# Performance work log

Hardware: AMD Instinct MI355X
Metric: run time of the kernel (lower is better)

Reference implementation:

```python
import jax, jax.numpy as jnp
import numpy as np

STATE_SIZE = 29
ACTION_SIZE = 3


def setup_inputs() -> dict:
    key = jax.random.key(0)
    ks = jax.random.split(key, 12)

    def row_norm(k, shape, scale=1.0):
        w = jax.random.normal(k, shape, dtype=jnp.float32)
        return w * (scale / jnp.sqrt(jnp.sum(w * w, axis=1, keepdims=True)))

    lrelu_gain = float(np.sqrt(2.0 / (1.0 + 0.01 ** 2)))  # torch calculate_gain('leaky_relu')
    inp = {
        "x": jax.random.normal(ks[0], (1, STATE_SIZE), dtype=jnp.float32),
        "hx": jnp.zeros((1, 128), jnp.float32),
        "cx": jnp.zeros((1, 128), jnp.float32),
        "w1": row_norm(ks[1], (256, STATE_SIZE)) * lrelu_gain,
        "b1": jnp.zeros((256,), jnp.float32),
        "w2": row_norm(ks[2], (256, 256)) * lrelu_gain,
        "b2": jnp.zeros((256,), jnp.float32),
        "w3": row_norm(ks[3], (128, 256)) * lrelu_gain,
        "b3": jnp.zeros((128,), jnp.float32),
        "w4": row_norm(ks[4], (128, 128)) * lrelu_gain,
        "b4": jnp.zeros((128,), jnp.float32),
        "w_ih": jax.random.normal(ks[5], (512, 128), dtype=jnp.float32) * 0.08,
        "b_ih": jnp.zeros((512,), jnp.float32),
        "w_hh": jax.random.normal(ks[6], (512, 128), dtype=jnp.float32) * 0.08,
        "b_hh": jnp.zeros((512,), jnp.float32),
        "w_critic": row_norm(ks[7], (1, 128), 1.0),
        "b_critic": jnp.zeros((1,), jnp.float32),
        "w_actor": row_norm(ks[8], (ACTION_SIZE, 128), 0.01),
        "b_actor": jnp.zeros((ACTION_SIZE,), jnp.float32),
        "w_actor2": row_norm(ks[9], (ACTION_SIZE, 128), 0.01),
        "b_actor2": jnp.zeros((ACTION_SIZE,), jnp.float32),
    }
    return inp


def _lrelu(v):
    return jnp.where(v > 0, v, 0.1 * v)


def reference(x, hx, cx, w1, b1, w2, b2, w3, b3, w4, b4,
              w_ih, b_ih, w_hh, b_hh,
              w_critic, b_critic, w_actor, b_actor, w_actor2, b_actor2):
    h = _lrelu(x @ w1.T + b1)
    h = _lrelu(h @ w2.T + b2)
    h = _lrelu(h @ w3.T + b3)
    h = _lrelu(h @ w4.T + b4)            # [1,128]
    # LSTMCell: gate order i, f, g, o (PyTorch convention)
    gates = h @ w_ih.T + b_ih + hx @ w_hh.T + b_hh  # [1,512]
    i, f, g, o = jnp.split(gates, 4, axis=-1)
    c_new = jax.nn.sigmoid(f) * cx + jax.nn.sigmoid(i) * jnp.tanh(g)
    h_new = jax.nn.sigmoid(o) * jnp.tanh(c_new)      # [1,128]
    value = jnp.squeeze(h_new @ w_critic.T + b_critic)          # scalar
    actor = jax.nn.soft_sign(h_new @ w_actor.T + b_actor)
    actor = jnp.squeeze(actor)                                   # [action_size]
    actor2 = jnp.squeeze(h_new @ w_actor2.T + b_actor2)         # [action_size]
    return (value, actor, actor2)
```

## Files before the change

kernel.cpp:

```cpp
#include <hip/hip_runtime.h>
#include <math.h>


#define NB   96
#define TPB  256
#define MAGIC 0x3A3C5A17u

#define H1_OFF 0
#define H2_OFF 256
#define H3_OFF 512
#define H4_OFF 640
#define GT_OFF 768

__device__ __forceinline__ float lrelu(float v) { return v > 0.f ? v : 0.1f * v; }
__device__ __forceinline__ float sigm(float v)  { return 1.f / (1.f + __expf(-v)); }
__device__ __forceinline__ float dot4(float4 a, float4 b) {
    return a.x * b.x + a.y * b.y + a.z * b.z + a.w * b.w;
}

__device__ __forceinline__ void send(unsigned long long* p, float v) {
    unsigned lo = __float_as_uint(v);
    unsigned long long pk = (unsigned long long)lo |
                            ((unsigned long long)(lo ^ MAGIC) << 32);
    __hip_atomic_store(p, pk, __ATOMIC_RELAXED, __HIP_MEMORY_SCOPE_AGENT);
}

__device__ __forceinline__ float recv(unsigned long long* p) {
    unsigned long long pk =
        __hip_atomic_load(p, __ATOMIC_RELAXED, __HIP_MEMORY_SCOPE_AGENT);
    unsigned lo = (unsigned)pk, hi = (unsigned)(pk >> 32);
    if ((lo ^ MAGIC) == hi) return __uint_as_float(lo);
    __builtin_amdgcn_s_sleep(4);
    for (;;) {
        pk = __hip_atomic_load(p, __ATOMIC_RELAXED, __HIP_MEMORY_SCOPE_AGENT);
        lo = (unsigned)pk; hi = (unsigned)(pk >> 32);
        if ((lo ^ MAGIC) == hi) return __uint_as_float(lo);
        __builtin_amdgcn_s_sleep(16);
    }
}

__global__ __launch_bounds__(TPB, 1) void a3c_fwd(
    const float* __restrict__ x, const float* __restrict__ hx, const float* __restrict__ cx,
    const float* __restrict__ w1, const float* __restrict__ b1,
    const float* __restrict__ w2, const float* __restrict__ b2,
    const float* __restrict__ w3, const float* __restrict__ b3,
    const float* __restrict__ w4, const float* __restrict__ b4,
    const float* __restrict__ w_ih, const float* __restrict__ b_ih,
    const float* __restrict__ w_hh, const float* __restrict__ b_hh,
    const float* __restrict__ w_critic, const float* __restrict__ b_critic,
    const float* __restrict__ w_actor, const float* __restrict__ b_actor,
    const float* __restrict__ w_actor2, const float* __restrict__ b_actor2,
    float* __restrict__ out, unsigned long long* __restrict__ wsp)
{
    const int blk = blockIdx.x, tid = threadIdx.x;

    if (blk < 8) {
        const int row = blk * 32 + (tid >> 3), sub = tid & 7;
        float a[4];
        #pragma unroll
        for (int j = 0; j < 4; ++j) {
            int c = sub * 4 + j;
            a[j] = (c < 29) ? w1[row * 29 + c] : 0.f;
        }
        const float bb1 = b1[row];

        __shared__ __align__(16) float x_s[32];
        __shared__ __align__(16) float head_s[896];
        __shared__ __align__(16) float hb_s[8];
        __shared__ __align__(16) float cx_s[128];
        __shared__ __align__(16) float gates_s[512];
        __shared__ __align__(16) float hn_s[128];

        if (tid < 32) x_s[tid] = (tid < 29) ? x[tid] : 0.f;
        if (blk == 0) {
            if (tid < 32)        ((float4*)head_s)[tid] = ((const float4*)w_critic)[tid];
            else if (tid < 128)  ((float4*)head_s)[tid] = ((const float4*)w_actor)[tid - 32];
            else if (tid < 224)  ((float4*)head_s)[tid] = ((const float4*)w_actor2)[tid - 128];
            else if (tid == 224) hb_s[0] = b_critic[0];
            else if (tid < 228)  hb_s[tid - 224] = b_actor[tid - 225];
            else if (tid < 231)  hb_s[tid - 224] = b_actor2[tid - 228];
            if (tid >= 64 && tid < 192) cx_s[tid - 64] = cx[tid - 64];
        }
        __syncthreads();

        {
            const float* xp = x_s + sub * 4;
            float s = a[0] * xp[0] + a[1] * xp[1] + a[2] * xp[2] + a[3] * xp[3];
            s += __shfl_xor(s, 1); s += __shfl_xor(s, 2); s += __shfl_xor(s, 4);
            if (sub == 0) send(wsp + H1_OFF + row, lrelu(s + bb1));
        }

        if (blk == 0) {
            gates_s[tid]       = recv(wsp + GT_OFF + tid);
            gates_s[tid + 256] = recv(wsp + GT_OFF + tid + 256);
            __syncthreads();
            if (tid < 128) {
                float ig = gates_s[tid];
                float fg = gates_s[tid + 128];
                float gg = gates_s[tid + 256];
                float og = gates_s[tid + 384];
                float c  = sigm(fg) * cx_s[tid] + sigm(ig) * tanhf(gg);
                hn_s[tid] = sigm(og) * tanhf(c);
            }
            __syncthreads();
            if (tid < 64) {
                #pragma unroll
                for (int o = 0; o < 7; ++o) {
                    const float* wrow = head_s + o * 128;
                    float s = hn_s[tid] * wrow[tid] + hn_s[tid + 64] * wrow[tid + 64];
                    #pragma unroll
                    for (int m = 1; m < 64; m <<= 1) s += __shfl_xor(s, m);
                    if (tid == 0) {
                        float r = s + hb_s[o];
                        if (o >= 1 && o <= 3) r = r / (1.f + fabsf(r));
                        out[o] = r;
                    }
                }
            }
        }
        return;
    }

    if (blk < 40) {
        const int row = (blk - 8) * 8 + (tid >> 5), p = tid & 31;
        float4 a0, a1v;
        {
            const float4* wp = (const float4*)(w2 + row * 256 + p * 8);
            a0 = wp[0]; a1v = wp[1];
        }
        const float bb2 = b2[row];

        __shared__ __align__(16) float h1_s[256];
        h1_s[tid] = recv(wsp + H1_OFF + tid);
        __syncthreads();

        const float4* hp = (const float4*)(h1_s + p * 8);
        float s = dot4(a0, hp[0]) + dot4(a1v, hp[1]);
        s += __shfl_xor(s, 1); s += __shfl_xor(s, 2);
        s += __shfl_xor(s, 4); s += __shfl_xor(s, 8);
        s += __shfl_xor(s, 16);
        if (p == 0) send(wsp + H2_OFF + row, lrelu(s + bb2));
        return;
    }

    if (blk < 56) {
        const int row = (blk - 40) * 8 + (tid >> 5), p = tid & 31;
        float4 a0, a1v;
        {
            const float4* wp = (const float4*)(w3 + row * 256 + p * 8);
            a0 = wp[0]; a1v = wp[1];
        }
        const float bb3 = b3[row];

        __shared__ __align__(16) float h2_s[256];
        h2_s[tid] = recv(wsp + H2_OFF + tid);
        __syncthreads();

        const float4* hp = (const float4*)(h2_s + p * 8);
        float s = dot4(a0, hp[0]) + dot4(a1v, hp[1]);
        s += __shfl_xor(s, 1); s += __shfl_xor(s, 2);
        s += __shfl_xor(s, 4); s += __shfl_xor(s, 8);
        s += __shfl_xor(s, 16);
        if (p == 0) send(wsp + H3_OFF + row, lrelu(s + bb3));
        return;
    }

    if (blk < 64) {
        const int row = (blk - 56) * 16 + (tid >> 4), p = tid & 15;
        float4 a0, a1v;
        {
            const float4* wp = (const float4*)(w4 + row * 128 + p * 8);
            a0 = wp[0]; a1v = wp[1];
        }
        const float bb4 = b4[row];

        __shared__ __align__(16) float h3_s[128];
        if (tid < 128) h3_s[tid] = recv(wsp + H3_OFF + tid);
        __syncthreads();

        const float4* hp = (const float4*)(h3_s + p * 8);
        float s = dot4(a0, hp[0]) + dot4(a1v, hp[1]);
        s += __shfl_xor(s, 1); s += __shfl_xor(s, 2);
        s += __shfl_xor(s, 4); s += __shfl_xor(s, 8);
        if (p == 0) send(wsp + H4_OFF + row, lrelu(s + bb4));
        return;
    }

    {
        const int row = (blk - 64) * 16 + (tid >> 4), p = tid & 15;
        float4 ah0, ah1;
        {
            const float4* wp = (const float4*)(w_hh + row * 128 + p * 8);
            ah0 = wp[0]; ah1 = wp[1];
        }
        float4 ai0, ai1;
        {
            const float4* wp = (const float4*)(w_ih + row * 128 + p * 8);
            ai0 = wp[0]; ai1 = wp[1];
        }
        const float bsum = b_ih[row] + b_hh[row];

        __shared__ __align__(16) float hx_s[128];
        __shared__ __align__(16) float h4_s[128];
        if (tid < 128) hx_s[tid] = hx[tid];
        __syncthreads();

        float g0;
        {
            const float4* hp = (const float4*)(hx_s + p * 8);
            float s = dot4(ah0, hp[0]) + dot4(ah1, hp[1]);
            s += __shfl_xor(s, 1); s += __shfl_xor(s, 2);
            s += __shfl_xor(s, 4); s += __shfl_xor(s, 8);
            g0 = s + bsum;
        }

        if (tid < 128) h4_s[tid] = recv(wsp + H4_OFF + tid);
        __syncthreads();

        {
            const float4* hp = (const float4*)(h4_s + p * 8);
            float s = dot4(ai0, hp[0]) + dot4(ai1, hp[1]);
            s += __shfl_xor(s, 1); s += __shfl_xor(s, 2);
            s += __shfl_xor(s, 4); s += __shfl_xor(s, 8);
            if (p == 0) send(wsp + GT_OFF + row, g0 + s);
        }
    }
}

extern "C" void kernel_launch(void* const* d_in, const int* in_sizes, int n_in,
                              void* d_out, int out_size, void* d_ws, size_t ws_size,
                              hipStream_t stream) {
    const float* x        = (const float*)d_in[0];
    const float* hx       = (const float*)d_in[1];
    const float* cx       = (const float*)d_in[2];
    const float* w1       = (const float*)d_in[3];
    const float* b1       = (const float*)d_in[4];
    const float* w2       = (const float*)d_in[5];
    const float* b2       = (const float*)d_in[6];
    const float* w3       = (const float*)d_in[7];
    const float* b3       = (const float*)d_in[8];
    const float* w4       = (const float*)d_in[9];
    const float* b4       = (const float*)d_in[10];
    const float* w_ih     = (const float*)d_in[11];
    const float* b_ih     = (const float*)d_in[12];
    const float* w_hh     = (const float*)d_in[13];
    const float* b_hh     = (const float*)d_in[14];
    const float* w_critic = (const float*)d_in[15];
    const float* b_critic = (const float*)d_in[16];
    const float* w_actor  = (const float*)d_in[17];
    const float* b_actor  = (const float*)d_in[18];
    const float* w_actor2 = (const float*)d_in[19];
    const float* b_actor2 = (const float*)d_in[20];
    float* out = (float*)d_out;
    unsigned long long* wsp = (unsigned long long*)d_ws;

    a3c_fwd<<<NB, TPB, 0, stream>>>(x, hx, cx, w1, b1, w2, b2, w3, b3, w4, b4,
                                    w_ih, b_ih, w_hh, b_hh,
                                    w_critic, b_critic, w_actor, b_actor,
                                    w_actor2, b_actor2, out, wsp);
}
```

Before: 103.1 us.

## Fuse layer4, LSTM gates and head partials into gate blocks to cut sync hops

Each of 32 LSTM blocks now recomputes the full layer-4 activation redundantly from h3, then computes its 4 cells' gates, the cell update, and partial head dot products. A single final block reduces those partials and writes the outputs. This removes two cross-block flag hops (h4 publish and gather of all gates into block 0), shortening the serial dependency chain. In exchange every gate block loads all of w4 into registers, which raises register pressure and redundant traffic, and the polling sleep intervals are also shortened.

```diff
diff --git a/kernel.cpp b/kernel.cpp
--- a/kernel.cpp
+++ b/kernel.cpp
@@ -2,15 +2,14 @@
 #include <math.h>
 
 
-#define NB   96
+#define NB   89
 #define TPB  256
 #define MAGIC 0x3A3C5A17u
 
 #define H1_OFF 0
 #define H2_OFF 256
 #define H3_OFF 512
-#define H4_OFF 640
-#define GT_OFF 768
+#define PT_OFF 640
 
 __device__ __forceinline__ float lrelu(float v) { return v > 0.f ? v : 0.1f * v; }
 __device__ __forceinline__ float sigm(float v)  { return 1.f / (1.f + __expf(-v)); }
@@ -24,18 +23,17 @@
                             ((unsigned long long)(lo ^ MAGIC) << 32);
     __hip_atomic_store(p, pk, __ATOMIC_RELAXED, __HIP_MEMORY_SCOPE_AGENT);
 }
-
 __device__ __forceinline__ float recv(unsigned long long* p) {
     unsigned long long pk =
         __hip_atomic_load(p, __ATOMIC_RELAXED, __HIP_MEMORY_SCOPE_AGENT);
     unsigned lo = (unsigned)pk, hi = (unsigned)(pk >> 32);
     if ((lo ^ MAGIC) == hi) return __uint_as_float(lo);
-    __builtin_amdgcn_s_sleep(4);
+    __builtin_amdgcn_s_sleep(2);
     for (;;) {
         pk = __hip_atomic_load(p, __ATOMIC_RELAXED, __HIP_MEMORY_SCOPE_AGENT);
         lo = (unsigned)pk; hi = (unsigned)(pk >> 32);
         if ((lo ^ MAGIC) == hi) return __uint_as_float(lo);
-        __builtin_amdgcn_s_sleep(16);
+        __builtin_amdgcn_s_sleep(8);
     }
 }
 
@@ -65,64 +63,121 @@
         const float bb1 = b1[row];
 
         __shared__ __align__(16) float x_s[32];
-        __shared__ __align__(16) float head_s[896];
+        if (tid < 32) x_s[tid] = (tid < 29) ? x[tid] : 0.f;
+        __syncthreads();
+
+        const float* xp = x_s + sub * 4;
+        float s = a[0] * xp[0] + a[1] * xp[1] + a[2] * xp[2] + a[3] * xp[3];
+        s += __shfl_xor(s, 1); s += __shfl_xor(s, 2); s += __shfl_xor(s, 4);
+        if (sub == 0) send(wsp + H1_OFF + row, lrelu(s + bb1));
+        return;
+    }
+
+    if (blk < 40) {
+        const int g  = blk - 8;
+        const int gc = g * 4;
+        const int r  = tid >> 4, p = tid & 15;
+        const int gate = r >> 2, cell = r & 3;
+        const int grow = gate * 128 + gc + cell;
+        const int r4 = tid >> 1, p4 = tid & 1;
+
+        __shared__ __align__(16) float hx_s[128];
+        __shared__ __align__(16) float h3_s[128];
+        __shared__ __align__(16) float h4_s[128];
+        __shared__ __align__(16) float g_s[16];
+        __shared__ __align__(16) float hn_s[4];
+        __shared__ __align__(16) float hw_s[28];
         __shared__ __align__(16) float hb_s[8];
-        __shared__ __align__(16) float cx_s[128];
-        __shared__ __align__(16) float gates_s[512];
-        __shared__ __align__(16) float hn_s[128];
-
-        if (tid < 32) x_s[tid] = (tid < 29) ? x[tid] : 0.f;
-        if (blk == 0) {
-            if (tid < 32)        ((float4*)head_s)[tid] = ((const float4*)w_critic)[tid];
-            else if (tid < 128)  ((float4*)head_s)[tid] = ((const float4*)w_actor)[tid - 32];
-            else if (tid < 224)  ((float4*)head_s)[tid] = ((const float4*)w_actor2)[tid - 128];
-            else if (tid == 224) hb_s[0] = b_critic[0];
-            else if (tid < 228)  hb_s[tid - 224] = b_actor[tid - 225];
-            else if (tid < 231)  hb_s[tid - 224] = b_actor2[tid - 228];
-            if (tid >= 64 && tid < 192) cx_s[tid - 64] = cx[tid - 64];
-        }
-        __syncthreads();
-
-        {
-            const float* xp = x_s + sub * 4;
-            float s = a[0] * xp[0] + a[1] * xp[1] + a[2] * xp[2] + a[3] * xp[3];
-            s += __shfl_xor(s, 1); s += __shfl_xor(s, 2); s += __shfl_xor(s, 4);
-            if (sub == 0) send(wsp + H1_OFF + row, lrelu(s + bb1));
-        }
-
-        if (blk == 0) {
-            gates_s[tid]       = recv(wsp + GT_OFF + tid);
-            gates_s[tid + 256] = recv(wsp + GT_OFF + tid + 256);
-            __syncthreads();
-            if (tid < 128) {
-                float ig = gates_s[tid];
-                float fg = gates_s[tid + 128];
-                float gg = gates_s[tid + 256];
-                float og = gates_s[tid + 384];
-                float c  = sigm(fg) * cx_s[tid] + sigm(ig) * tanhf(gg);
-                hn_s[tid] = sigm(og) * tanhf(c);
-            }
-            __syncthreads();
-            if (tid < 64) {
-                #pragma unroll
-                for (int o = 0; o < 7; ++o) {
-                    const float* wrow = head_s + o * 128;
-                    float s = hn_s[tid] * wrow[tid] + hn_s[tid + 64] * wrow[tid + 64];
-                    #pragma unroll
-                    for (int m = 1; m < 64; m <<= 1) s += __shfl_xor(s, m);
-                    if (tid == 0) {
-                        float r = s + hb_s[o];
-                        if (o >= 1 && o <= 3) r = r / (1.f + fabsf(r));
-                        out[o] = r;
-                    }
-                }
-            }
-        }
-        return;
-    }
-
-    if (blk < 40) {
-        const int row = (blk - 8) * 8 + (tid >> 5), p = tid & 31;
+
+        float4 ah0, ah1;
+        {
+            const float4* wp = (const float4*)(w_hh + grow * 128 + p * 8);
+            ah0 = wp[0]; ah1 = wp[1];
+        }
+        float4 a4[16];
+        {
+            const float4* wp = (const float4*)(w4 + r4 * 128 + p4 * 64);
+            #pragma unroll
+            for (int j = 0; j < 16; ++j) a4[j] = wp[j];
+        }
+        float4 ai0, ai1;
+        {
+            const float4* wp = (const float4*)(w_ih + grow * 128 + p * 8);
+            ai0 = wp[0]; ai1 = wp[1];
+        }
+        const float bsum = b_ih[grow] + b_hh[grow];
+        const float bb4  = b4[r4];
+        float cxv = (tid < 4) ? cx[gc + tid] : 0.f;
+
+        if (tid < 128) hx_s[tid] = hx[tid];
+        if (tid < 28) {
+            int o = tid >> 2, c = tid & 3;
+            float v;
+            if (o == 0)      v = w_critic[gc + c];
+            else if (o < 4)  v = w_actor [(o - 1) * 128 + gc + c];
+            else             v = w_actor2[(o - 4) * 128 + gc + c];
+            hw_s[tid] = v;
+        }
+        if (g == 0) {
+            if (tid == 224)      hb_s[0] = b_critic[0];
+            else if (tid < 228 && tid > 224) hb_s[tid - 224] = b_actor[tid - 225];
+            else if (tid >= 228 && tid < 231) hb_s[tid - 224] = b_actor2[tid - 228];
+        }
+        __syncthreads();
+
+        float g0;
+        {
+            const float4* hp = (const float4*)(hx_s + p * 8);
+            float s = dot4(ah0, hp[0]) + dot4(ah1, hp[1]);
+            s += __shfl_xor(s, 1); s += __shfl_xor(s, 2);
+            s += __shfl_xor(s, 4); s += __shfl_xor(s, 8);
+            g0 = s + bsum;
+        }
+
+        if (tid < 128) h3_s[tid] = recv(wsp + H3_OFF + tid);
+        __syncthreads();
+
+        {
+            const float4* hp = (const float4*)(h3_s + p4 * 64);
+            float s = 0.f;
+            #pragma unroll
+            for (int j = 0; j < 16; ++j) s += dot4(a4[j], hp[j]);
+            s += __shfl_xor(s, 1);
+            if (p4 == 0) h4_s[r4] = lrelu(s + bb4);
+        }
+        __syncthreads();
+
+        {
+            const float4* hp = (const float4*)(h4_s + p * 8);
+            float s = dot4(ai0, hp[0]) + dot4(ai1, hp[1]);
+            s += __shfl_xor(s, 1); s += __shfl_xor(s, 2);
+            s += __shfl_xor(s, 4); s += __shfl_xor(s, 8);
+            if (p == 0) g_s[r] = g0 + s;
+        }
+        __syncthreads();
+
+        if (tid < 4) {
+            float ig = g_s[tid];
+            float fg = g_s[4 + tid];
+            float gg = g_s[8 + tid];
+            float og = g_s[12 + tid];
+            float c  = sigm(fg) * cxv + sigm(ig) * tanhf(gg);
+            hn_s[tid] = sigm(og) * tanhf(c);
+        }
+        __syncthreads();
+
+        if (tid < 7) {
+            const float* wc = hw_s + tid * 4;
+            float s = wc[0] * hn_s[0] + wc[1] * hn_s[1]
+                    + wc[2] * hn_s[2] + wc[3] * hn_s[3];
+            if (g == 0) s += hb_s[tid];
+            send(wsp + PT_OFF + tid * 32 + g, s);
+        }
+        return;
+    }
+
+    if (blk < 72) {
+        const int row = (blk - 40) * 8 + (tid >> 5), p = tid & 31;
         float4 a0, a1v;
         {
             const float4* wp = (const float4*)(w2 + row * 256 + p * 8);
@@ -143,8 +198,8 @@
         return;
     }
 
-    if (blk < 56) {
-        const int row = (blk - 40) * 8 + (tid >> 5), p = tid & 31;
+    if (blk < 88) {
+        const int row = (blk - 72) * 8 + (tid >> 5), p = tid & 31;
         float4 a0, a1v;
         {
             const float4* wp = (const float4*)(w3 + row * 256 + p * 8);
@@ -165,64 +220,16 @@
         return;
     }
 
-    if (blk < 64) {
-        const int row = (blk - 56) * 16 + (tid >> 4), p = tid & 15;
-        float4 a0, a1v;
-        {
-            const float4* wp = (const float4*)(w4 + row * 128 + p * 8);
-            a0 = wp[0]; a1v = wp[1];
-        }
-        const float bb4 = b4[row];
-
-        __shared__ __align__(16) float h3_s[128];
-        if (tid < 128) h3_s[tid] = recv(wsp + H3_OFF + tid);
-        __syncthreads();
-
-        const float4* hp = (const float4*)(h3_s + p * 8);
-        float s = dot4(a0, hp[0]) + dot4(a1v, hp[1]);
+    if (tid < 224) {
+        float s = recv(wsp + PT_OFF + tid);
+        const int o = tid >> 5, k = tid & 31;
         s += __shfl_xor(s, 1); s += __shfl_xor(s, 2);
         s += __shfl_xor(s, 4); s += __shfl_xor(s, 8);
-        if (p == 0) send(wsp + H4_OFF + row, lrelu(s + bb4));
-        return;
-    }
-
-    {
-        const int row = (blk - 64) * 16 + (tid >> 4), p = tid & 15;
-        float4 ah0, ah1;
-        {
-            const float4* wp = (const float4*)(w_hh + row * 128 + p * 8);
-            ah0 = wp[0]; ah1 = wp[1];
-        }
-        float4 ai0, ai1;
-        {
-            const float4* wp = (const float4*)(w_ih + row * 128 + p * 8);
-            ai0 = wp[0]; ai1 = wp[1];
-        }
-        const float bsum = b_ih[row] + b_hh[row];
-
-        __shared__ __align__(16) float hx_s[128];
-        __shared__ __align__(16) float h4_s[128];
-        if (tid < 128) hx_s[tid] = hx[tid];
-        __syncthreads();
-
-        float g0;
-        {
-            const float4* hp = (const float4*)(hx_s + p * 8);
-            float s = dot4(ah0, hp[0]) + dot4(ah1, hp[1]);
-            s += __shfl_xor(s, 1); s += __shfl_xor(s, 2);
-            s += __shfl_xor(s, 4); s += __shfl_xor(s, 8);
-            g0 = s + bsum;
-        }
-
-        if (tid < 128) h4_s[tid] = recv(wsp + H4_OFF + tid);
-        __syncthreads();
-
-        {
-            const float4* hp = (const float4*)(h4_s + p * 8);
-            float s = dot4(ai0, hp[0]) + dot4(ai1, hp[1]);
-            s += __shfl_xor(s, 1); s += __shfl_xor(s, 2);
-            s += __shfl_xor(s, 4); s += __shfl_xor(s, 8);
-            if (p == 0) send(wsp + GT_OFF + row, g0 + s);
+        s += __shfl_xor(s, 16);
+        if (k == 0) {
+            float r = s;
+            if (o >= 1 && o <= 3) r = r / (1.f + fabsf(r));
+            out[o] = r;
         }
     }
 }
```

Result: no change. 102.1 us (-1.0%).
